# Kernel tuning notes

Measured on AMD Instinct MI355X. Metric: run time of the kernel, lower is better.

## Reference

```python
import jax, jax.numpy as jnp
import numpy as np

N = 20000       # nodes
E = 320000      # edges
D_IN = 128
H = 512
OUT = 7
EPS = 1e-5


def setup_inputs() -> dict:
    key = jax.random.key(0)
    ks = jax.random.split(key, 16)
    def lin(k, fan_in, fan_out):
        bound = 1.0 / np.sqrt(fan_in)
        kw, kb = jax.random.split(k)
        W = jax.random.uniform(kw, (fan_in, fan_out), jnp.float32, -bound, bound)
        b = jax.random.uniform(kb, (fan_out,), jnp.float32, -bound, bound)
        return W, b
    x = jax.random.normal(ks[0], (N, D_IN), jnp.float32)
    edge_index = jax.random.randint(ks[1], (2, E), 0, N, dtype=jnp.int64)
    W1, b1 = lin(ks[2], D_IN, H)
    W2, b2 = lin(ks[3], H, H)
    W3, b3 = lin(ks[4], H, H)
    W4, b4 = lin(ks[5], H, H)
    ln_gamma = jnp.ones((H,), jnp.float32)
    ln_beta = jnp.zeros((H,), jnp.float32)
    W_out, b_out = lin(ks[6], H, OUT)
    return {"x": x, "edge_index": edge_index,
            "W1": W1, "b1": b1, "W2": W2, "b2": b2,
            "W3": W3, "b3": b3, "W4": W4, "b4": b4,
            "ln_gamma": ln_gamma, "ln_beta": ln_beta,
            "W_out": W_out, "b_out": b_out}


def _gcn_layer(x, W, b, src, dst, dinv):
    # transform, then symmetric-normalized gather/scatter-add (PyG GCNConv)
    h = x @ W                                    # [N, H]
    norm = dinv[src] * dinv[dst]                 # [E+N]
    msg = h[src] * norm[:, None]                 # gather + scale
    agg = jax.ops.segment_sum(msg, dst, num_segments=N)
    return agg + b


def reference(x, edge_index, W1, b1, W2, b2, W3, b3, W4, b4,
              ln_gamma, ln_beta, W_out, b_out):
    loops = jnp.arange(N, dtype=edge_index.dtype)
    src = jnp.concatenate([edge_index[0], loops])  # A + I self loops
    dst = jnp.concatenate([edge_index[1], loops])
    deg = jax.ops.segment_sum(jnp.ones_like(src, dtype=x.dtype), dst,
                              num_segments=N)
    dinv = jnp.where(deg > 0, jax.lax.rsqrt(deg), 0.0)

    def ln(h):
        mu = h.mean(-1, keepdims=True)
        var = h.var(-1, keepdims=True)
        return (h - mu) * jax.lax.rsqrt(var + EPS) * ln_gamma + ln_beta

    for W, b in ((W1, b1), (W2, b2), (W3, b3), (W4, b4)):
        x = jax.nn.relu(ln(_gcn_layer(x, W, b, src, dst, dinv)))
    g = x.mean(axis=0)           # mean pool over nodes -> [H]
    # dropout is identity in eval mode
    return g @ W_out + b_out     # [OUT]
```

## Files before the change

kernel.cpp:

```cpp
#include <hip/hip_runtime.h>

#define HID 512
#define OUTD 7
#define EPSV 1e-5f
#define PB 256
#define PR 32

typedef __attribute__((ext_vector_type(8))) short bf16x8;
typedef __attribute__((ext_vector_type(4))) float f32x4;
typedef __attribute__((ext_vector_type(2))) float f32x2;
typedef unsigned short ushort_t;
typedef unsigned int uint_t;
typedef unsigned char uchar_t;

__device__ __forceinline__ ushort_t f2bf(float f) {
    uint_t u = __float_as_uint(f);
    u = (u + 0x7fffu + ((u >> 16) & 1u)) >> 16;
    return (ushort_t)u;
}
__device__ __forceinline__ float bflo(uint_t u) { return __uint_as_float(u << 16); }
__device__ __forceinline__ float bfhi(uint_t u) { return __uint_as_float(u & 0xffff0000u); }

__device__ __forceinline__ void dec4(uint_t v, float* f) {
    f32x2 p0 = __builtin_amdgcn_cvt_pk_f32_fp8(v, false);
    f32x2 p1 = __builtin_amdgcn_cvt_pk_f32_fp8(v, true);
    f[0] = p0.x; f[1] = p0.y; f[2] = p1.x; f[3] = p1.y;
}
__device__ __forceinline__ uint_t enc4(float a, float b, float c, float d) {
    uint_t r = __builtin_amdgcn_cvt_pk_fp8_f32(a, b, 0, false);
    r = __builtin_amdgcn_cvt_pk_fp8_f32(c, d, r, true);
    return r;
}

__device__ __forceinline__ void gload_lds16(const ushort_t* g, ushort_t* l) {
    __builtin_amdgcn_global_load_lds(
        (const __attribute__((address_space(1))) uint_t*)g,
        (__attribute__((address_space(3))) uint_t*)l, 16, 0, 0);
}

__global__ __launch_bounds__(256) void deg_wtrans(
        const int* __restrict__ dst, int* __restrict__ deg, int E, int degB,
        const float* __restrict__ W0, const float* __restrict__ W1,
        const float* __restrict__ W2, const float* __restrict__ W3,
        ushort_t* __restrict__ T0, ushort_t* __restrict__ T1,
        ushort_t* __restrict__ T2, ushort_t* __restrict__ T3) {
    __shared__ ushort_t tile[32][33];
    if ((int)blockIdx.x < degB) {
        int e = blockIdx.x * 256 + threadIdx.x;
        if (e < E) atomicAdd(&deg[dst[e]], 1);
        return;
    }
    int id = blockIdx.x - degB;
    const float* W; ushort_t* T; int K;
    if (id < 64)       { W = W0; T = T0; K = 128; }
    else if (id < 320) { W = W1; T = T1; K = 512; id -= 64; }
    else if (id < 576) { W = W2; T = T2; K = 512; id -= 320; }
    else               { W = W3; T = T3; K = 512; id -= 576; }
    const int tn = id & 15;
    const int tk = id >> 4;
    const int t = threadIdx.x;
    const int r = t >> 3;
    const int c4 = (t & 7) * 4;
    const float4 v = *(const float4*)&W[(size_t)(tk * 32 + r) * HID + tn * 32 + c4];
    tile[r][c4 + 0] = f2bf(v.x); tile[r][c4 + 1] = f2bf(v.y);
    tile[r][c4 + 2] = f2bf(v.z); tile[r][c4 + 3] = f2bf(v.w);
    __syncthreads();
    ushort4 ov = make_ushort4(tile[c4 + 0][r], tile[c4 + 1][r],
                              tile[c4 + 2][r], tile[c4 + 3][r]);
    *(ushort4*)&T[(size_t)(tn * 32 + r) * K + tk * 32 + c4] = ov;
}


__global__ void scan1(const int* __restrict__ deg, int* __restrict__ off,
                      int* __restrict__ partial, float* __restrict__ dinv, int N) {
    __shared__ int s[256];
    const int t = threadIdx.x;
    const int i = blockIdx.x * 256 + t;
    int d = (i < N) ? deg[i] : 0;
    if (i < N) dinv[i] = rsqrtf((float)(d + 1));
    s[t] = d;
    __syncthreads();
#pragma unroll
    for (int ofs = 1; ofs < 256; ofs <<= 1) {
        int v = (t >= ofs) ? s[t - ofs] : 0;
        __syncthreads();
        s[t] += v;
        __syncthreads();
    }
    if (i < N) off[i] = s[t] - d;
    if (t == 255) partial[blockIdx.x] = s[255];
}

__global__ void scan23(int* __restrict__ off, const int* __restrict__ partial,
                       int* __restrict__ cursor, int N, int E, int nb) {
    __shared__ int s[256];
    __shared__ int ex[256];
    const int t = threadIdx.x;
    int d = (t < nb) ? partial[t] : 0;
    s[t] = d;
    __syncthreads();
#pragma unroll
    for (int ofs = 1; ofs < 256; ofs <<= 1) {
        int v = (t >= ofs) ? s[t - ofs] : 0;
        __syncthreads();
        s[t] += v;
        __syncthreads();
    }
    ex[t] = s[t] - d;
    __syncthreads();
    int i = blockIdx.x * 256 + t;
    if (i < N) {
        int v = off[i] + ex[i >> 8];
        off[i] = v;
        cursor[i] = v;
    } else if (i == N) {
        off[N] = E;
    }
}


__global__ void fill_cvt(const int* __restrict__ src, const int* __restrict__ dst,
                         int* __restrict__ cursor, int* __restrict__ srcs, int E,
                         const float* __restrict__ x, const float* __restrict__ dinv,
                         ushort_t* __restrict__ xb, int pairs) {
    int i = blockIdx.x * blockDim.x + threadIdx.x;
    if (i < E) { int p = atomicAdd(&cursor[dst[i]], 1); srcs[p] = src[i]; return; }
    i -= E;
    if (i < pairs) {
        float dr = dinv[i >> 6];
        float a = x[2 * i] * dr, b = x[2 * i + 1] * dr;
        uint_t d = __builtin_amdgcn_cvt_pk_fp8_f32(a, b, 0, false);
        xb[i] = (ushort_t)(d & 0xffffu);
    }
}


__global__ __launch_bounds__(256) void csr_agg_512(
        const uchar_t* __restrict__ xs, const int* __restrict__ off,
        const int* __restrict__ srcs, const float* __restrict__ dinv,
        ushort_t* __restrict__ ax, int N) {
    int gtid = blockIdx.x * 256 + threadIdx.x;
    int r = gtid >> 6, lane = gtid & 63;
    if (r >= N) return;
    const int half = lane >> 5, l32 = lane & 31;
    const uint4* xb = (const uint4*)xs;
    float a[16];
    if (half == 0) {
        uint4 v = xb[(size_t)r * 32 + l32];
        dec4(v.x, a); dec4(v.y, a + 4); dec4(v.z, a + 8); dec4(v.w, a + 12);
    } else {
#pragma unroll
        for (int q = 0; q < 16; q++) a[q] = 0.f;
    }
    int e = off[r];
    const int e1 = off[r + 1];
    for (; e + 8 <= e1; e += 8) {
        int si[4]; uint4 vi[4];
#pragma unroll
        for (int j = 0; j < 4; j++) si[j] = srcs[e + 2 * j + half];
#pragma unroll
        for (int j = 0; j < 4; j++) vi[j] = xb[(size_t)si[j] * 32 + l32];
#pragma unroll
        for (int j = 0; j < 4; j++) {
            float f[16];
            dec4(vi[j].x, f); dec4(vi[j].y, f + 4); dec4(vi[j].z, f + 8); dec4(vi[j].w, f + 12);
#pragma unroll
            for (int q = 0; q < 16; q++) a[q] += f[q];
        }
    }
    for (; e < e1; e += 2) {
        int idx = e + half;
        bool valid = idx < e1;
        int s = srcs[valid ? idx : e];
        uint4 v = xb[(size_t)s * 32 + l32];
        if (!valid) { v.x = 0; v.y = 0; v.z = 0; v.w = 0; }
        float f[16];
        dec4(v.x, f); dec4(v.y, f + 4); dec4(v.z, f + 8); dec4(v.w, f + 12);
#pragma unroll
        for (int q = 0; q < 16; q++) a[q] += f[q];
    }
#pragma unroll
    for (int q = 0; q < 16; q++) a[q] += __shfl_xor(a[q], 32);
    {
        float dr = dinv[r];
        const int b = half * 8;
        uint_t w0 = (uint_t)f2bf(a[b + 0] * dr) | ((uint_t)f2bf(a[b + 1] * dr) << 16);
        uint_t w1 = (uint_t)f2bf(a[b + 2] * dr) | ((uint_t)f2bf(a[b + 3] * dr) << 16);
        uint_t w2 = (uint_t)f2bf(a[b + 4] * dr) | ((uint_t)f2bf(a[b + 5] * dr) << 16);
        uint_t w3 = (uint_t)f2bf(a[b + 6] * dr) | ((uint_t)f2bf(a[b + 7] * dr) << 16);
        ((uint4*)ax)[(size_t)r * 64 + l32 * 2 + half] = make_uint4(w0, w1, w2, w3);
    }
}

__global__ __launch_bounds__(256) void csr_agg_128(
        const uchar_t* __restrict__ xs, const int* __restrict__ off,
        const int* __restrict__ srcs, const float* __restrict__ dinv,
        ushort_t* __restrict__ ax, int N) {
    int gtid = blockIdx.x * 256 + threadIdx.x;
    int r = gtid >> 6, lane = gtid & 63;
    if (r >= N) return;
    const int sub = lane >> 3, l8 = lane & 7;
    const uint4* xb = (const uint4*)xs;
    float a[16];
    if (sub == 0) {
        uint4 v = xb[(size_t)r * 8 + l8];
        dec4(v.x, a); dec4(v.y, a + 4); dec4(v.z, a + 8); dec4(v.w, a + 12);
    } else {
#pragma unroll
        for (int q = 0; q < 16; q++) a[q] = 0.f;
    }
    const int e1 = off[r + 1];
    for (int e = off[r]; e < e1; e += 8) {
        int idx = e + sub;
        bool valid = idx < e1;
        int s = srcs[valid ? idx : e];
        uint4 v = xb[(size_t)s * 8 + l8];
        if (!valid) { v.x = 0; v.y = 0; v.z = 0; v.w = 0; }
        float f[16];
        dec4(v.x, f); dec4(v.y, f + 4); dec4(v.z, f + 8); dec4(v.w, f + 12);
#pragma unroll
        for (int q = 0; q < 16; q++) a[q] += f[q];
    }
#pragma unroll
    for (int q = 0; q < 16; q++) a[q] += __shfl_xor(a[q], 8);
#pragma unroll
    for (int q = 0; q < 16; q++) a[q] += __shfl_xor(a[q], 16);
#pragma unroll
    for (int q = 0; q < 16; q++) a[q] += __shfl_xor(a[q], 32);
    if (sub < 2) {
        float dr = dinv[r];
        const int b = sub * 8;
        uint_t w0 = (uint_t)f2bf(a[b + 0] * dr) | ((uint_t)f2bf(a[b + 1] * dr) << 16);
        uint_t w1 = (uint_t)f2bf(a[b + 2] * dr) | ((uint_t)f2bf(a[b + 3] * dr) << 16);
        uint_t w2 = (uint_t)f2bf(a[b + 4] * dr) | ((uint_t)f2bf(a[b + 5] * dr) << 16);
        uint_t w3 = (uint_t)f2bf(a[b + 6] * dr) | ((uint_t)f2bf(a[b + 7] * dr) << 16);
        ((uint4*)ax)[(size_t)r * 16 + l8 * 2 + sub] = make_uint4(w0, w1, w2, w3);
    }
}


__global__ __launch_bounds__(256) void gemm_mfma(
        const ushort_t* __restrict__ A, const ushort_t* __restrict__ Wt,
        const float* __restrict__ bias, ushort_t* __restrict__ C, int M, int K, int MB) {
    __shared__ __align__(16) ushort_t AsL[128 * 64];
    __shared__ __align__(16) ushort_t BsL[128 * 64];
    const int id = blockIdx.x;
    const int mb = (id >> 5) * 8 + (id & 7);
    const int nbk = (id >> 3) & 3;
    if (mb >= MB) return;
    const int t = threadIdx.x;
    const int wave = t >> 6, lane = t & 63;
    const int m0 = mb * 128, n0 = nbk * 128;
    const int wm = (wave & 1) * 64, wn = (wave >> 1) * 64;
    const int quad = lane >> 4, l16 = lane & 15;
    const int srow = lane >> 3;
    const int schunk = (lane & 7) ^ srow;
    const int sw = (l16 & 7) << 4;

    f32x4 acc[4][4];
#pragma unroll
    for (int i = 0; i < 4; i++)
#pragma unroll
        for (int j = 0; j < 4; j++) acc[i][j] = (f32x4){0.f, 0.f, 0.f, 0.f};

    for (int k0 = 0; k0 < K; k0 += 64) {
#pragma unroll
        for (int j = 0; j < 4; j++) {
            const int c = wave * 4 + j;
            int gm = m0 + 8 * c + srow;
            if (gm >= M) gm = M - 1;
            gload_lds16(A + (size_t)gm * K + k0 + (schunk << 3), AsL + c * 512);
            gload_lds16(Wt + (size_t)(n0 + 8 * c + srow) * K + k0 + (schunk << 3),
                        BsL + c * 512);
        }
        __syncthreads();
#pragma unroll
        for (int kk = 0; kk < 2; kk++) {
            const int kb = (kk * 4 + quad) << 4;
            bf16x8 af[4], bfr[4];
#pragma unroll
            for (int jn = 0; jn < 4; jn++)
                bfr[jn] = *(const bf16x8*)((const char*)BsL
                              + (wn + jn * 16 + l16) * 128 + (kb ^ sw));
#pragma unroll
            for (int i = 0; i < 4; i++)
                af[i] = *(const bf16x8*)((const char*)AsL
                              + (wm + i * 16 + l16) * 128 + (kb ^ sw));
#pragma unroll
            for (int i = 0; i < 4; i++)
#pragma unroll
                for (int jn = 0; jn < 4; jn++)
                    acc[i][jn] = __builtin_amdgcn_mfma_f32_16x16x32_bf16(
                                     af[i], bfr[jn], acc[i][jn], 0, 0, 0);
        }
        __syncthreads();
    }
#pragma unroll
    for (int i = 0; i < 4; i++) {
#pragma unroll
        for (int jn = 0; jn < 4; jn++) {
            int gn = n0 + wn + jn * 16 + l16;
            float bv = bias[gn];
#pragma unroll
            for (int rg = 0; rg < 4; rg++) {
                int gm = m0 + wm + i * 16 + quad * 4 + rg;
                if (gm < M) C[(size_t)gm * HID + gn] = f2bf(acc[i][jn][rg] + bv);
            }
        }
    }
}


__global__ void ln_relu(const ushort_t* __restrict__ h, const float* __restrict__ gamma,
                        const float* __restrict__ beta, const float* __restrict__ dinv,
                        void* __restrict__ optr, int N) {
    int gtid = blockIdx.x * blockDim.x + threadIdx.x;
    int r = gtid >> 6, lane = gtid & 63;
    if (r >= N) return;
    uint4 v = ((const uint4*)(h + (size_t)r * HID))[lane];
    float f[8] = {bflo(v.x), bfhi(v.x), bflo(v.y), bfhi(v.y),
                  bflo(v.z), bfhi(v.z), bflo(v.w), bfhi(v.w)};
    float s = 0.f, q = 0.f;
#pragma unroll
    for (int j = 0; j < 8; j++) { s += f[j]; q += f[j] * f[j]; }
#pragma unroll
    for (int ofs = 32; ofs > 0; ofs >>= 1) {
        s += __shfl_xor(s, ofs);
        q += __shfl_xor(q, ofs);
    }
    float mu  = s * (1.0f / HID);
    float var = q * (1.0f / HID) - mu * mu;
    float rs  = rsqrtf(var + EPSV);
    float dr  = dinv[r];
    const float4* gp = (const float4*)gamma;
    const float4* bp = (const float4*)beta;
    float4 g0 = gp[2 * lane], g1 = gp[2 * lane + 1];
    float4 b0 = bp[2 * lane], b1 = bp[2 * lane + 1];
    float gg[8] = {g0.x, g0.y, g0.z, g0.w, g1.x, g1.y, g1.z, g1.w};
    float bb[8] = {b0.x, b0.y, b0.z, b0.w, b1.x, b1.y, b1.z, b1.w};
    float o[8];
#pragma unroll
    for (int j = 0; j < 8; j++)
        o[j] = fmaxf((f[j] - mu) * rs * gg[j] + bb[j], 0.f) * dr;
    uint2 ov;
    ov.x = enc4(o[0], o[1], o[2], o[3]);
    ov.y = enc4(o[4], o[5], o[6], o[7]);
    ((uint2*)optr)[(size_t)r * 64 + lane] = ov;
}


__global__ __launch_bounds__(256) void ln_pool(
        const ushort_t* __restrict__ h, const float* __restrict__ gamma,
        const float* __restrict__ beta, float* __restrict__ pbuf, int N) {
    __shared__ float sred[4][64][8];
    const int t = threadIdx.x;
    const int sub = t >> 6, lane = t & 63;
    const float4* gp = (const float4*)gamma;
    const float4* bp = (const float4*)beta;
    float4 g0 = gp[2 * lane], g1 = gp[2 * lane + 1];
    float4 b0 = bp[2 * lane], b1 = bp[2 * lane + 1];
    float gg[8] = {g0.x, g0.y, g0.z, g0.w, g1.x, g1.y, g1.z, g1.w};
    float bb[8] = {b0.x, b0.y, b0.z, b0.w, b1.x, b1.y, b1.z, b1.w};
    float colacc[8] = {0.f, 0.f, 0.f, 0.f, 0.f, 0.f, 0.f, 0.f};
    const int step = PB * 4;
    for (int r = blockIdx.x * 4 + sub; r < N; r += step) {
        uint4 v = ((const uint4*)(h + (size_t)r * HID))[lane];
        float f[8] = {bflo(v.x), bfhi(v.x), bflo(v.y), bfhi(v.y),
                      bflo(v.z), bfhi(v.z), bflo(v.w), bfhi(v.w)};
        float s = 0.f, q = 0.f;
#pragma unroll
        for (int j = 0; j < 8; j++) { s += f[j]; q += f[j] * f[j]; }
#pragma unroll
        for (int ofs = 32; ofs > 0; ofs >>= 1) {
            s += __shfl_xor(s, ofs);
            q += __shfl_xor(q, ofs);
        }
        float mu  = s * (1.0f / HID);
        float var = q * (1.0f / HID) - mu * mu;
        float rs  = rsqrtf(var + EPSV);
#pragma unroll
        for (int j = 0; j < 8; j++)
            colacc[j] += fmaxf((f[j] - mu) * rs * gg[j] + bb[j], 0.f);
    }
#pragma unroll
    for (int j = 0; j < 8; j++) sred[sub][lane][j] = colacc[j];
    __syncthreads();
    if (sub == 0) {
        float4 o0, o1;
        o0.x = sred[0][lane][0] + sred[1][lane][0] + sred[2][lane][0] + sred[3][lane][0];
        o0.y = sred[0][lane][1] + sred[1][lane][1] + sred[2][lane][1] + sred[3][lane][1];
        o0.z = sred[0][lane][2] + sred[1][lane][2] + sred[2][lane][2] + sred[3][lane][2];
        o0.w = sred[0][lane][3] + sred[1][lane][3] + sred[2][lane][3] + sred[3][lane][3];
        o1.x = sred[0][lane][4] + sred[1][lane][4] + sred[2][lane][4] + sred[3][lane][4];
        o1.y = sred[0][lane][5] + sred[1][lane][5] + sred[2][lane][5] + sred[3][lane][5];
        o1.z = sred[0][lane][6] + sred[1][lane][6] + sred[2][lane][6] + sred[3][lane][6];
        o1.w = sred[0][lane][7] + sred[1][lane][7] + sred[2][lane][7] + sred[3][lane][7];
        float* pb = pbuf + (size_t)blockIdx.x * HID + lane * 8;
        ((float4*)pb)[0] = o0;
        ((float4*)pb)[1] = o1;
    }
}


__global__ __launch_bounds__(256) void pool_reduce(
        const float* __restrict__ pbuf, float* __restrict__ pbuf2) {
    const int t = threadIdx.x;
    const int b = blockIdx.x;
    const int R = PB / PR;
    float2 s = make_float2(0.f, 0.f);
#pragma unroll
    for (int u = 0; u < R; u++) {
        const float2 v = ((const float2*)(pbuf + (size_t)(b * R + u) * HID))[t];
        s.x += v.x; s.y += v.y;
    }
    ((float2*)(pbuf2 + (size_t)b * HID))[t] = s;
}


__global__ void out_kernel(const float* __restrict__ pbuf2, const float* __restrict__ Wout,
                           const float* __restrict__ bout, float* __restrict__ out, int N) {
    __shared__ float red[256];
    int t = threadIdx.x;
    float g0 = 0.f, g1 = 0.f;
#pragma unroll
    for (int p = 0; p < PR; p += 8) {
#pragma unroll
        for (int u = 0; u < 8; u++) {
            const float2 v = ((const float2*)(pbuf2 + (size_t)(p + u) * HID))[t];
            g0 += v.x; g1 += v.y;
        }
    }
    float invn = 1.0f / (float)N;
    for (int o = 0; o < OUTD; o++) {
        float pr = g0 * Wout[(2 * t) * OUTD + o] + g1 * Wout[(2 * t + 1) * OUTD + o];
        red[t] = pr;
        __syncthreads();
        for (int sft = 128; sft > 0; sft >>= 1) {
            if (t < sft) red[t] += red[t + sft];
            __syncthreads();
        }
        if (t == 0) out[o] = red[0] * invn + bout[o];
        __syncthreads();
    }
}


extern "C" void kernel_launch(void* const* d_in, const int* in_sizes, int n_in,
                              void* d_out, int out_size, void* d_ws, size_t ws_size,
                              hipStream_t stream) {
    const float* x  = (const float*)d_in[0];
    const int*   ei = (const int*)d_in[1];
    const int N = in_sizes[0] / 128;
    const int E = in_sizes[1] / 2;
    const int* src = ei;
    const int* dst = ei + E;
    const float* Ws[4] = {(const float*)d_in[2], (const float*)d_in[4],
                          (const float*)d_in[6], (const float*)d_in[8]};
    const float* bs[4] = {(const float*)d_in[3], (const float*)d_in[5],
                          (const float*)d_in[7], (const float*)d_in[9]};
    const float* gamma = (const float*)d_in[10];
    const float* beta  = (const float*)d_in[11];
    const float* Wout  = (const float*)d_in[12];
    const float* bout  = (const float*)d_in[13];
    float* out = (float*)d_out;

    char* p = (char*)d_ws;
    ushort_t* axb = (ushort_t*)p;  p += sizeof(ushort_t) * (size_t)N * HID;
    ushort_t* hb  = (ushort_t*)p;  p += sizeof(ushort_t) * (size_t)N * HID;
    uchar_t*  ho8 = (uchar_t*)p;   p += (size_t)N * HID;
    uchar_t*  xb8 = ho8;
    ushort_t* Wt[4];
    Wt[0] = (ushort_t*)p;          p += sizeof(ushort_t) * 128 * HID;
    Wt[1] = (ushort_t*)p;          p += sizeof(ushort_t) * HID * HID;
    Wt[2] = (ushort_t*)p;          p += sizeof(ushort_t) * HID * HID;
    Wt[3] = (ushort_t*)p;          p += sizeof(ushort_t) * HID * HID;
    float* dinv  = (float*)p;      p += sizeof(float) * N;
    float* pbuf  = (float*)p;      p += sizeof(float) * PB * HID;
    float* pbuf2 = (float*)p;      p += sizeof(float) * PR * HID;
    int* deg    = (int*)p;         p += sizeof(int) * N;
    int* off    = (int*)p;         p += sizeof(int) * (N + 4);
    int* cursor = (int*)p;         p += sizeof(int) * N;
    int* partial= (int*)p;         p += sizeof(int) * 256;
    int* srcs   = (int*)p;

    const int nb = (N + 255) / 256;
    const int MB = (N + 127) / 128;
    const int gemm_blocks = 32 * ((MB + 7) / 8);
    const int degB = (E + 255) / 256;

    hipMemsetAsync(deg, 0, sizeof(int) * N, stream);
    deg_wtrans<<<degB + 832, 256, 0, stream>>>(dst, deg, E, degB,
                                               Ws[0], Ws[1], Ws[2], Ws[3],
                                               Wt[0], Wt[1], Wt[2], Wt[3]);
    scan1<<<nb, 256, 0, stream>>>(deg, off, partial, dinv, N);
    scan23<<<(N + 256) / 256, 256, 0, stream>>>(off, partial, cursor, N, E, nb);
    {
        int pairs = N * 64;
        int tot = E + pairs;
        fill_cvt<<<(tot + 255) / 256, 256, 0, stream>>>(src, dst, cursor, srcs, E,
                                                        x, dinv, (ushort_t*)xb8, pairs);
    }

    for (int l = 0; l < 4; l++) {
        const int K = (l == 0) ? 128 : HID;
        if (l == 0)
            csr_agg_128<<<(N * 64 + 255) / 256, 256, 0, stream>>>(xb8, off, srcs, dinv, axb, N);
        else
            csr_agg_512<<<(N * 64 + 255) / 256, 256, 0, stream>>>(ho8, off, srcs, dinv, axb, N);
        gemm_mfma<<<gemm_blocks, 256, 0, stream>>>(axb, Wt[l], bs[l], hb, N, K, MB);
        if (l < 3)
            ln_relu<<<(N * 64 + 255) / 256, 256, 0, stream>>>(hb, gamma, beta, dinv, ho8, N);
        else
            ln_pool<<<PB, 256, 0, stream>>>(hb, gamma, beta, pbuf, N);
    }
    pool_reduce<<<PR, 256, 0, stream>>>(pbuf, pbuf2);
    out_kernel<<<1, 256, 0, stream>>>(pbuf2, Wout, bout, out, N);
}
```

Before: 362.1 us.

## Fuse LayerNorm/ReLU and mean-pool epilogue into full-width GEMM kernel

The GEMM is retiled so each block computes 32 full rows of 512 outputs, with the whole weight slab staged in LDS. That lets LayerNorm statistics be reduced inside the block and the normalized, ReLU'd, dinv-scaled fp8 output be written directly. The separate bf16 intermediate buffer, the ln_relu kernel and the ln_pool kernel are removed, and the last layer accumulates per-block column sums for pooling. The trade-off is that every block reloads all of W per k-step (64KB of LDS for B), which gives lower occupancy and more L2 traffic for weights, and the A tile is only 32 rows.

New measurement: 426.2 us. 1.18x slower.

```diff
diff --git a/kernel.cpp b/kernel.cpp
--- a/kernel.cpp
+++ b/kernel.cpp
@@ -3,7 +3,6 @@
 #define HID 512
 #define OUTD 7
 #define EPSV 1e-5f
-#define PB 256
 #define PR 32
 
 typedef __attribute__((ext_vector_type(8))) short bf16x8;
@@ -239,179 +238,161 @@
 }
 
 
-__global__ __launch_bounds__(256) void gemm_mfma(
+template<int POOL>
+__global__ __launch_bounds__(256) void gemm_ln(
         const ushort_t* __restrict__ A, const ushort_t* __restrict__ Wt,
-        const float* __restrict__ bias, ushort_t* __restrict__ C, int M, int K, int MB) {
-    __shared__ __align__(16) ushort_t AsL[128 * 64];
-    __shared__ __align__(16) ushort_t BsL[128 * 64];
-    const int id = blockIdx.x;
-    const int mb = (id >> 5) * 8 + (id & 7);
-    const int nbk = (id >> 3) & 3;
-    if (mb >= MB) return;
+        const float* __restrict__ bias, const float* __restrict__ gamma,
+        const float* __restrict__ beta, const float* __restrict__ dinv,
+        uchar_t* __restrict__ out8, float* __restrict__ pbuf, int M, int K) {
+    __shared__ __align__(16) ushort_t AsL[32 * 64];
+    __shared__ __align__(16) ushort_t BsL[512 * 64];
+    __shared__ float sred[4][32][2];
     const int t = threadIdx.x;
     const int wave = t >> 6, lane = t & 63;
-    const int m0 = mb * 128, n0 = nbk * 128;
-    const int wm = (wave & 1) * 64, wn = (wave >> 1) * 64;
+    const int m0 = blockIdx.x * 32;
+    const int wn = wave * 128;
     const int quad = lane >> 4, l16 = lane & 15;
     const int srow = lane >> 3;
     const int schunk = (lane & 7) ^ srow;
     const int sw = (l16 & 7) << 4;
 
-    f32x4 acc[4][4];
-#pragma unroll
-    for (int i = 0; i < 4; i++)
-#pragma unroll
-        for (int j = 0; j < 4; j++) acc[i][j] = (f32x4){0.f, 0.f, 0.f, 0.f};
+    f32x4 acc[2][8];
+#pragma unroll
+    for (int im = 0; im < 2; im++)
+#pragma unroll
+        for (int jn = 0; jn < 8; jn++) acc[im][jn] = (f32x4){0.f, 0.f, 0.f, 0.f};
 
     for (int k0 = 0; k0 < K; k0 += 64) {
-#pragma unroll
-        for (int j = 0; j < 4; j++) {
-            const int c = wave * 4 + j;
-            int gm = m0 + 8 * c + srow;
+        {
+            int gm = m0 + wave * 8 + srow;
             if (gm >= M) gm = M - 1;
-            gload_lds16(A + (size_t)gm * K + k0 + (schunk << 3), AsL + c * 512);
-            gload_lds16(Wt + (size_t)(n0 + 8 * c + srow) * K + k0 + (schunk << 3),
+            gload_lds16(A + (size_t)gm * K + k0 + (schunk << 3), AsL + wave * 512);
+        }
+#pragma unroll
+        for (int j = 0; j < 16; j++) {
+            const int c = wave * 16 + j;
+            gload_lds16(Wt + (size_t)(8 * c + srow) * K + k0 + (schunk << 3),
                         BsL + c * 512);
         }
         __syncthreads();
 #pragma unroll
         for (int kk = 0; kk < 2; kk++) {
             const int kb = (kk * 4 + quad) << 4;
-            bf16x8 af[4], bfr[4];
-#pragma unroll
-            for (int jn = 0; jn < 4; jn++)
+            bf16x8 af[2], bfr[8];
+#pragma unroll
+            for (int jn = 0; jn < 8; jn++)
                 bfr[jn] = *(const bf16x8*)((const char*)BsL
                               + (wn + jn * 16 + l16) * 128 + (kb ^ sw));
 #pragma unroll
-            for (int i = 0; i < 4; i++)
-                af[i] = *(const bf16x8*)((const char*)AsL
-                              + (wm + i * 16 + l16) * 128 + (kb ^ sw));
-#pragma unroll
-            for (int i = 0; i < 4; i++)
-#pragma unroll
-                for (int jn = 0; jn < 4; jn++)
-                    acc[i][jn] = __builtin_amdgcn_mfma_f32_16x16x32_bf16(
-                                     af[i], bfr[jn], acc[i][jn], 0, 0, 0);
-        }
-        __syncthreads();
-    }
-#pragma unroll
-    for (int i = 0; i < 4; i++) {
-#pragma unroll
-        for (int jn = 0; jn < 4; jn++) {
-            int gn = n0 + wn + jn * 16 + l16;
-            float bv = bias[gn];
+            for (int im = 0; im < 2; im++)
+                af[im] = *(const bf16x8*)((const char*)AsL
+                              + (im * 16 + l16) * 128 + (kb ^ sw));
+#pragma unroll
+            for (int im = 0; im < 2; im++)
+#pragma unroll
+                for (int jn = 0; jn < 8; jn++)
+                    acc[im][jn] = __builtin_amdgcn_mfma_f32_16x16x32_bf16(
+                                      bfr[jn], af[im], acc[im][jn], 0, 0, 0);
+        }
+        __syncthreads();
+    }
+
+    float4 bias4[8];
+#pragma unroll
+    for (int jn = 0; jn < 8; jn++)
+        bias4[jn] = *(const float4*)&bias[wn + jn * 16 + quad * 4];
+
+#pragma unroll
+    for (int im = 0; im < 2; im++) {
+        float s = 0.f, q = 0.f;
+#pragma unroll
+        for (int jn = 0; jn < 8; jn++) {
 #pragma unroll
             for (int rg = 0; rg < 4; rg++) {
-                int gm = m0 + wm + i * 16 + quad * 4 + rg;
-                if (gm < M) C[(size_t)gm * HID + gn] = f2bf(acc[i][jn][rg] + bv);
+                float h = acc[im][jn][rg] + ((const float*)&bias4[jn])[rg];
+                s += h; q += h * h;
             }
         }
-    }
-}
-
-
-__global__ void ln_relu(const ushort_t* __restrict__ h, const float* __restrict__ gamma,
-                        const float* __restrict__ beta, const float* __restrict__ dinv,
-                        void* __restrict__ optr, int N) {
-    int gtid = blockIdx.x * blockDim.x + threadIdx.x;
-    int r = gtid >> 6, lane = gtid & 63;
-    if (r >= N) return;
-    uint4 v = ((const uint4*)(h + (size_t)r * HID))[lane];
-    float f[8] = {bflo(v.x), bfhi(v.x), bflo(v.y), bfhi(v.y),
-                  bflo(v.z), bfhi(v.z), bflo(v.w), bfhi(v.w)};
-    float s = 0.f, q = 0.f;
-#pragma unroll
-    for (int j = 0; j < 8; j++) { s += f[j]; q += f[j] * f[j]; }
-#pragma unroll
-    for (int ofs = 32; ofs > 0; ofs >>= 1) {
-        s += __shfl_xor(s, ofs);
-        q += __shfl_xor(q, ofs);
-    }
-    float mu  = s * (1.0f / HID);
-    float var = q * (1.0f / HID) - mu * mu;
-    float rs  = rsqrtf(var + EPSV);
-    float dr  = dinv[r];
-    const float4* gp = (const float4*)gamma;
-    const float4* bp = (const float4*)beta;
-    float4 g0 = gp[2 * lane], g1 = gp[2 * lane + 1];
-    float4 b0 = bp[2 * lane], b1 = bp[2 * lane + 1];
-    float gg[8] = {g0.x, g0.y, g0.z, g0.w, g1.x, g1.y, g1.z, g1.w};
-    float bb[8] = {b0.x, b0.y, b0.z, b0.w, b1.x, b1.y, b1.z, b1.w};
-    float o[8];
-#pragma unroll
-    for (int j = 0; j < 8; j++)
-        o[j] = fmaxf((f[j] - mu) * rs * gg[j] + bb[j], 0.f) * dr;
-    uint2 ov;
-    ov.x = enc4(o[0], o[1], o[2], o[3]);
-    ov.y = enc4(o[4], o[5], o[6], o[7]);
-    ((uint2*)optr)[(size_t)r * 64 + lane] = ov;
-}
-
-
-__global__ __launch_bounds__(256) void ln_pool(
-        const ushort_t* __restrict__ h, const float* __restrict__ gamma,
-        const float* __restrict__ beta, float* __restrict__ pbuf, int N) {
-    __shared__ float sred[4][64][8];
-    const int t = threadIdx.x;
-    const int sub = t >> 6, lane = t & 63;
-    const float4* gp = (const float4*)gamma;
-    const float4* bp = (const float4*)beta;
-    float4 g0 = gp[2 * lane], g1 = gp[2 * lane + 1];
-    float4 b0 = bp[2 * lane], b1 = bp[2 * lane + 1];
-    float gg[8] = {g0.x, g0.y, g0.z, g0.w, g1.x, g1.y, g1.z, g1.w};
-    float bb[8] = {b0.x, b0.y, b0.z, b0.w, b1.x, b1.y, b1.z, b1.w};
-    float colacc[8] = {0.f, 0.f, 0.f, 0.f, 0.f, 0.f, 0.f, 0.f};
-    const int step = PB * 4;
-    for (int r = blockIdx.x * 4 + sub; r < N; r += step) {
-        uint4 v = ((const uint4*)(h + (size_t)r * HID))[lane];
-        float f[8] = {bflo(v.x), bfhi(v.x), bflo(v.y), bfhi(v.y),
-                      bflo(v.z), bfhi(v.z), bflo(v.w), bfhi(v.w)};
-        float s = 0.f, q = 0.f;
-#pragma unroll
-        for (int j = 0; j < 8; j++) { s += f[j]; q += f[j] * f[j]; }
-#pragma unroll
-        for (int ofs = 32; ofs > 0; ofs >>= 1) {
-            s += __shfl_xor(s, ofs);
-            q += __shfl_xor(q, ofs);
-        }
-        float mu  = s * (1.0f / HID);
-        float var = q * (1.0f / HID) - mu * mu;
-        float rs  = rsqrtf(var + EPSV);
-#pragma unroll
-        for (int j = 0; j < 8; j++)
-            colacc[j] += fmaxf((f[j] - mu) * rs * gg[j] + bb[j], 0.f);
-    }
-#pragma unroll
-    for (int j = 0; j < 8; j++) sred[sub][lane][j] = colacc[j];
+        s += __shfl_xor(s, 16); s += __shfl_xor(s, 32);
+        q += __shfl_xor(q, 16); q += __shfl_xor(q, 32);
+        if (quad == 0) { sred[wave][im * 16 + l16][0] = s; sred[wave][im * 16 + l16][1] = q; }
+    }
     __syncthreads();
-    if (sub == 0) {
-        float4 o0, o1;
-        o0.x = sred[0][lane][0] + sred[1][lane][0] + sred[2][lane][0] + sred[3][lane][0];
-        o0.y = sred[0][lane][1] + sred[1][lane][1] + sred[2][lane][1] + sred[3][lane][1];
-        o0.z = sred[0][lane][2] + sred[1][lane][2] + sred[2][lane][2] + sred[3][lane][2];
-        o0.w = sred[0][lane][3] + sred[1][lane][3] + sred[2][lane][3] + sred[3][lane][3];
-        o1.x = sred[0][lane][4] + sred[1][lane][4] + sred[2][lane][4] + sred[3][lane][4];
-        o1.y = sred[0][lane][5] + sred[1][lane][5] + sred[2][lane][5] + sred[3][lane][5];
-        o1.z = sred[0][lane][6] + sred[1][lane][6] + sred[2][lane][6] + sred[3][lane][6];
-        o1.w = sred[0][lane][7] + sred[1][lane][7] + sred[2][lane][7] + sred[3][lane][7];
-        float* pb = pbuf + (size_t)blockIdx.x * HID + lane * 8;
-        ((float4*)pb)[0] = o0;
-        ((float4*)pb)[1] = o1;
+
+    float cacc[8][4];
+    if (POOL) {
+#pragma unroll
+        for (int jn = 0; jn < 8; jn++)
+#pragma unroll
+            for (int rg = 0; rg < 4; rg++) cacc[jn][rg] = 0.f;
+    }
+
+#pragma unroll
+    for (int im = 0; im < 2; im++) {
+        const int row = im * 16 + l16;
+        const float st = sred[0][row][0] + sred[1][row][0] + sred[2][row][0] + sred[3][row][0];
+        const float qt = sred[0][row][1] + sred[1][row][1] + sred[2][row][1] + sred[3][row][1];
+        const float mu = st * (1.0f / HID);
+        const float var = qt * (1.0f / HID) - mu * mu;
+        const float rs = rsqrtf(var + EPSV);
+        const int gm = m0 + row;
+        const bool ok = gm < M;
+        float dr = 0.f;
+        if (!POOL) dr = ok ? dinv[gm] : 0.f;
+#pragma unroll
+        for (int jn = 0; jn < 8; jn++) {
+            const float4 g4 = *(const float4*)&gamma[wn + jn * 16 + quad * 4];
+            const float4 b4 = *(const float4*)&beta[wn + jn * 16 + quad * 4];
+            float o[4];
+#pragma unroll
+            for (int rg = 0; rg < 4; rg++) {
+                float h = acc[im][jn][rg] + ((const float*)&bias4[jn])[rg];
+                o[rg] = fmaxf((h - mu) * rs * ((const float*)&g4)[rg]
+                              + ((const float*)&b4)[rg], 0.f);
+            }
+            if (POOL) {
+#pragma unroll
+                for (int rg = 0; rg < 4; rg++) cacc[jn][rg] += ok ? o[rg] : 0.f;
+            } else if (ok) {
+                *(uint_t*)(out8 + (size_t)gm * HID + wn + jn * 16 + quad * 4) =
+                    enc4(o[0] * dr, o[1] * dr, o[2] * dr, o[3] * dr);
+            }
+        }
+    }
+
+    if (POOL) {
+#pragma unroll
+        for (int jn = 0; jn < 8; jn++)
+#pragma unroll
+            for (int rg = 0; rg < 4; rg++) {
+                float v = cacc[jn][rg];
+                v += __shfl_xor(v, 1); v += __shfl_xor(v, 2);
+                v += __shfl_xor(v, 4); v += __shfl_xor(v, 8);
+                cacc[jn][rg] = v;
+            }
+        if (l16 == 0) {
+#pragma unroll
+            for (int jn = 0; jn < 8; jn++) {
+                float4 v = make_float4(cacc[jn][0], cacc[jn][1], cacc[jn][2], cacc[jn][3]);
+                *(float4*)&pbuf[(size_t)blockIdx.x * HID + wn + jn * 16 + quad * 4] = v;
+            }
+        }
     }
 }
 
 
 __global__ __launch_bounds__(256) void pool_reduce(
-        const float* __restrict__ pbuf, float* __restrict__ pbuf2) {
+        const float* __restrict__ pbuf, float* __restrict__ pbuf2, int NB) {
     const int t = threadIdx.x;
     const int b = blockIdx.x;
-    const int R = PB / PR;
+    const int R = (NB + PR - 1) / PR;
     float2 s = make_float2(0.f, 0.f);
-#pragma unroll
     for (int u = 0; u < R; u++) {
-        const float2 v = ((const float2*)(pbuf + (size_t)(b * R + u) * HID))[t];
-        s.x += v.x; s.y += v.y;
+        int r = b * R + u;
+        if (r < NB) {
+            const float2 v = ((const float2*)(pbuf + (size_t)r * HID))[t];
+            s.x += v.x; s.y += v.y;
+        }
     }
     ((float2*)(pbuf2 + (size_t)b * HID))[t] = s;
 }
@@ -464,9 +445,10 @@
     const float* bout  = (const float*)d_in[13];
     float* out = (float*)d_out;
 
+    const int NBM = (N + 31) / 32;
+
     char* p = (char*)d_ws;
     ushort_t* axb = (ushort_t*)p;  p += sizeof(ushort_t) * (size_t)N * HID;
-    ushort_t* hb  = (ushort_t*)p;  p += sizeof(ushort_t) * (size_t)N * HID;
     uchar_t*  ho8 = (uchar_t*)p;   p += (size_t)N * HID;
     uchar_t*  xb8 = ho8;
     ushort_t* Wt[4];
@@ -475,7 +457,7 @@
     Wt[2] = (ushort_t*)p;          p += sizeof(ushort_t) * HID * HID;
     Wt[3] = (ushort_t*)p;          p += sizeof(ushort_t) * HID * HID;
     float* dinv  = (float*)p;      p += sizeof(float) * N;
-    float* pbuf  = (float*)p;      p += sizeof(float) * PB * HID;
+    float* pbuf  = (float*)p;      p += sizeof(float) * (size_t)(NBM + 4) * HID;
     float* pbuf2 = (float*)p;      p += sizeof(float) * PR * HID;
     int* deg    = (int*)p;         p += sizeof(int) * N;
     int* off    = (int*)p;         p += sizeof(int) * (N + 4);
@@ -484,8 +466,6 @@
     int* srcs   = (int*)p;
 
     const int nb = (N + 255) / 256;
-    const int MB = (N + 127) / 128;
-    const int gemm_blocks = 32 * ((MB + 7) / 8);
     const int degB = (E + 255) / 256;
 
     hipMemsetAsync(deg, 0, sizeof(int) * N, stream);
@@ -507,12 +487,13 @@
             csr_agg_128<<<(N * 64 + 255) / 256, 256, 0, stream>>>(xb8, off, srcs, dinv, axb, N);
         else
             csr_agg_512<<<(N * 64 + 255) / 256, 256, 0, stream>>>(ho8, off, srcs, dinv, axb, N);
-        gemm_mfma<<<gemm_blocks, 256, 0, stream>>>(axb, Wt[l], bs[l], hb, N, K, MB);
         if (l < 3)
-            ln_relu<<<(N * 64 + 255) / 256, 256, 0, stream>>>(hb, gamma, beta, dinv, ho8, N);
+            gemm_ln<0><<<NBM, 256, 0, stream>>>(axb, Wt[l], bs[l], gamma, beta, dinv,
+                                                ho8, pbuf, N, K);
         else
-            ln_pool<<<PB, 256, 0, stream>>>(hb, gamma, beta, pbuf, N);
-    }
-    pool_reduce<<<PR, 256, 0, stream>>>(pbuf, pbuf2);
+            gemm_ln<1><<<NBM, 256, 0, stream>>>(axb, Wt[l], bs[l], gamma, beta, dinv,
+                                                ho8, pbuf, N, K);
+    }
+    pool_reduce<<<PR, 256, 0, stream>>>(pbuf, pbuf2, NBM);
     out_kernel<<<1, 256, 0, stream>>>(pbuf2, Wout, bout, out, N);
 }
```
